# Kernel tuning notes

Hardware: AMD Instinct MI355X
Metric: run time of the kernel (lower is better)

## Reference

```python
import jax, jax.numpy as jnp
import numpy as np

D_FEAT = 6
HID = 256
T = 60
B_DAYS = 4
STOCKS = 512
TRAIN_DAYS = 240
K_DAY = 10
N_NEIGHBOR = 10
SLOPE = 0.01  # nn.LeakyReLU default


def setup_inputs() -> dict:
    key = jax.random.key(0)
    ks = jax.random.split(key, 32)
    g = lambda i, shape, s=0.05: (jax.random.normal(ks[i], shape, dtype=jnp.float32) * s)
    inp = jax.random.normal(ks[0], (B_DAYS, STOCKS, D_FEAT * T), dtype=jnp.float32)
    train_hidden = jax.random.normal(ks[1], (TRAIN_DAYS, STOCKS, HID), dtype=jnp.float32)
    train_hidden_day = jax.random.normal(ks[2], (TRAIN_DAYS, HID), dtype=jnp.float32)
    return {
        "inp": inp,
        "train_hidden": train_hidden,
        "train_hidden_day": train_hidden_day,
        # GRU layer 0 (input D_FEAT) and layer 1 (input HID); gates [r,z,n] stacked -> 3*HID
        "W_ih0": g(3, (3 * HID, D_FEAT)), "W_hh0": g(4, (3 * HID, HID)),
        "b_ih0": g(5, (3 * HID,)), "b_hh0": g(6, (3 * HID,)),
        "W_ih1": g(7, (3 * HID, HID)), "W_hh1": g(8, (3 * HID, HID)),
        "b_ih1": g(9, (3 * HID,)), "b_hh1": g(10, (3 * HID,)),
        # lins MLP 256->512->512->256
        "lin0_W": g(11, (512, HID)), "lin0_b": g(12, (512,)),
        "lin1_W": g(13, (512, 512)), "lin1_b": g(14, (512,)),
        "lin2_W": g(15, (HID, 512)), "lin2_b": g(16, (HID,)),
        # projections (no bias) and output head
        "proj1_W": g(17, (HID, HID)), "proj2_W": g(18, (HID, HID)),
        "fc_W": g(19, (1, 2 * HID)), "fc_b": g(20, (1,)),
    }


def _leaky(x):
    return jnp.where(x >= 0, x, SLOPE * x)


def _gru_layer(x, W_ih, W_hh, b_ih, b_hh):
    # x: [N, T, in] -> [N, T, HID]
    xW = jnp.einsum('nti,gi->ntg', x, W_ih) + b_ih  # precompute input gates
    def step(h, xw):
        gh = h @ W_hh.T + b_hh
        xr, xz, xn = jnp.split(xw, 3, axis=-1)
        hr, hz, hn = jnp.split(gh, 3, axis=-1)
        r = jax.nn.sigmoid(xr + hr)
        z = jax.nn.sigmoid(xz + hz)
        n = jnp.tanh(xn + r * hn)
        h = (1.0 - z) * n + z * h
        return h, h
    h0 = jnp.zeros((x.shape[0], W_hh.shape[1]), x.dtype)
    _, hs = jax.lax.scan(step, h0, jnp.swapaxes(xW, 0, 1))
    return jnp.swapaxes(hs, 0, 1)


def _cos_sim(x, y):
    xy = x @ y.T
    xn = jnp.sqrt(jnp.sum(x * x, axis=1))[:, None]
    yn = jnp.sqrt(jnp.sum(y * y, axis=1))[:, None]
    cs = xy / (xn @ yn.T)
    return jnp.where(jnp.isnan(cs), 0.0, cs)


def reference(inp, train_hidden, train_hidden_day,
              W_ih0, W_hh0, b_ih0, b_hh0, W_ih1, W_hh1, b_ih1, b_hh1,
              lin0_W, lin0_b, lin1_W, lin1_b, lin2_W, lin2_b,
              proj1_W, proj2_W, fc_W, fc_b):
    B, S = inp.shape[0], inp.shape[1]
    x = inp.reshape(B * S, D_FEAT, -1).transpose(0, 2, 1)  # [N, T, d_feat]
    h = _gru_layer(x, W_ih0, W_hh0, b_ih0, b_hh0)
    h = _gru_layer(h, W_ih1, W_hh1, b_ih1, b_hh1)
    out = h[:, -1, :]                                      # [N, HID]
    mb = _leaky(out @ lin0_W.T + lin0_b)
    mb = _leaky(mb @ lin1_W.T + lin1_b)
    mb = _leaky(mb @ lin2_W.T + lin2_b)                    # mini_batch_out [N, HID]
    mb_day = jnp.mean(mb.reshape(B, S, -1), axis=1)        # [B, HID]
    day_sim = _cos_sim(mb_day, train_hidden_day)           # [B, TRAIN_DAYS]
    _, day_idx = jax.lax.top_k(day_sim, K_DAY)             # [B, K_DAY]
    sample = train_hidden[day_idx].reshape(-1, train_hidden.shape[-1])  # [B*K_DAY*S, HID]
    q = mb @ proj1_W.T
    kh = sample @ proj2_W.T
    cs = _cos_sim(q, kh)                                   # [N, B*K_DAY*S]
    vals, idx = jax.lax.top_k(cs, N_NEIGHBOR)              # per-row top-k (distinct cols)
    # sparse mask (ones/n_neighbor) * cos_sim, then sparse @ kh == weighted gather-sum
    agg = jnp.einsum('nk,nkh->nh', vals / N_NEIGHBOR, kh[idx])
    cat = jnp.concatenate([mb, agg], axis=1)               # [N, 2*HID]
    y = (cat @ fc_W.T + fc_b).squeeze(-1)
    return y.reshape(B, -1)
```

## Files before the change

### kernel.cpp

```cpp
#include <hip/hip_runtime.h>
#include <cmath>
#include <cstdint>

#define D_FEAT 6
#define T_SEQ  60
#define HID    256
#define G3     768
#define NROW   2048
#define NSAMP  20480

__device__ __forceinline__ float sigmoidf_(float x) { return 1.0f / (1.0f + expf(-x)); }

struct PrepArgs {
  const float* src[9];
  float* dst[9];
  int N[9], K[9], ro[9];
};

__global__ void prep_weights(PrepArgs a) {
  int seg = blockIdx.y;
  const float* S = a.src[seg];
  float* D = a.dst[seg];
  int N = a.N[seg], K = a.K[seg], ro = a.ro[seg];
  int total = N * K;
  for (int i = blockIdx.x * blockDim.x + threadIdx.x; i < total; i += gridDim.x * blockDim.x) {
    int n = i / K, k = i - n * K;
    D[(size_t)(k + ro) * N + n] = S[i];
  }
}

__device__ __forceinline__ void kloop128(const float* __restrict__ A,
                                         const float* __restrict__ B,
                                         float (&acc)[3][8])
{
  float4 Aa[4][2];
  float  Bb[2][12];
#pragma unroll
  for (int c = 0; c < 4; ++c) {
    Aa[c][0] = *(const float4*)(A + c * 8);
    Aa[c][1] = *(const float4*)(A + c * 8 + 4);
  }
#pragma unroll
  for (int c = 0; c < 4; ++c)
#pragma unroll
    for (int u = 0; u < 3; ++u)
      Bb[0][c * 3 + u] = B[(size_t)c * G3 + u * 256];

  for (int kb = 0; kb < 128; kb += 8) {
    {
      const float* p = B + (size_t)(kb + 4) * G3;
#pragma unroll
      for (int c = 0; c < 4; ++c)
#pragma unroll
        for (int u = 0; u < 3; ++u)
          Bb[1][c * 3 + u] = p[(size_t)c * G3 + u * 256];
    }
#pragma unroll
    for (int c = 0; c < 4; ++c) {
      float4 alo = Aa[c][0], ahi = Aa[c][1];
      int kn = kb + 4 + c;
      Aa[c][0] = *(const float4*)(A + kn * 8);
      Aa[c][1] = *(const float4*)(A + kn * 8 + 4);
#pragma unroll
      for (int u = 0; u < 3; ++u) {
        float b = Bb[0][c * 3 + u];
        acc[u][0] += alo.x * b; acc[u][1] += alo.y * b;
        acc[u][2] += alo.z * b; acc[u][3] += alo.w * b;
        acc[u][4] += ahi.x * b; acc[u][5] += ahi.y * b;
        acc[u][6] += ahi.z * b; acc[u][7] += ahi.w * b;
      }
    }
    {
      int kw = (kb + 8) & 127;
      const float* p = B + (size_t)kw * G3;
#pragma unroll
      for (int c = 0; c < 4; ++c)
#pragma unroll
        for (int u = 0; u < 3; ++u)
          Bb[0][c * 3 + u] = p[(size_t)c * G3 + u * 256];
    }
#pragma unroll
    for (int c = 0; c < 4; ++c) {
      float4 alo = Aa[c][0], ahi = Aa[c][1];
      int kn = (kb + 8 + c) & 127;
      Aa[c][0] = *(const float4*)(A + kn * 8);
      Aa[c][1] = *(const float4*)(A + kn * 8 + 4);
#pragma unroll
      for (int u = 0; u < 3; ++u) {
        float b = Bb[1][c * 3 + u];
        acc[u][0] += alo.x * b; acc[u][1] += alo.y * b;
        acc[u][2] += alo.z * b; acc[u][3] += alo.w * b;
        acc[u][4] += ahi.x * b; acc[u][5] += ahi.y * b;
        acc[u][6] += ahi.z * b; acc[u][7] += ahi.w * b;
      }
    }
  }
}

__global__ __launch_bounds__(512, 1)
void gru_fused(const float* __restrict__ inp, const float* __restrict__ WThh0,
               const float* __restrict__ WTcat, const float* __restrict__ WTih0,
               const float* __restrict__ bih0, const float* __restrict__ bhh0,
               const float* __restrict__ bih1, const float* __restrict__ bhh1,
               float* __restrict__ hrow)
{
  __shared__ float h0A[2048], h0B[2048];
  __shared__ float h1A[2048], h1B[2048];
  __shared__ float xls[2880];
  __shared__ float exch[256 * 33];

  const int tid = threadIdx.x;
  const int col = tid & 255;
  const int half = tid >> 8;
  const int m0 = blockIdx.x * 8;

  for (int c = tid; c < 2880; c += 512) {
    int row = c / 360, it = c - row * 360;
    xls[it * 8 + row] = inp[(size_t)(m0 + row) * 360 + it];
  }
  for (int c = tid; c < 2048; c += 512) { h0A[c] = 0.f; h1A[c] = 0.f; }

  float h0c[8], h1c[8];
#pragma unroll
  for (int r = 0; r < 8; ++r) { h0c[r] = 0.f; h1c[r] = 0.f; }

  float b_ih0[3], b_hh0[3], b_ih1[3], b_hh1[3];
#pragma unroll
  for (int u = 0; u < 3; ++u) {
    int o = u * 256 + col;
    b_ih0[u] = bih0[o]; b_hh0[u] = bhh0[o];
    b_ih1[u] = bih1[o]; b_hh1[u] = bhh1[o];
  }
  __syncthreads();

  const int aoff = half * 1024;
  const float* Bhh0 = WThh0 + (size_t)(half * 128) * G3 + col;
  const float* Bc0  = WTcat + (size_t)(half * 128) * G3 + col;
  const float* Bc1  = WTcat + (size_t)(256 + half * 128) * G3 + col;
  float* exc = exch + col * 33;

  for (int t = 0; t < T_SEQ; ++t) {
    const float* h0cur = (t & 1) ? h0B : h0A;
    float*       h0nxt = (t & 1) ? h0A : h0B;
    const float* h1cur = (t & 1) ? h1B : h1A;
    float*       h1nxt = (t & 1) ? h1A : h1B;

    float gh[3][8];
#pragma unroll
    for (int u = 0; u < 3; ++u)
#pragma unroll
      for (int r = 0; r < 8; ++r) gh[u][r] = 0.f;
    kloop128(h0cur + aoff, Bhh0, gh);

    float xw[3][8];
    if (half == 0) {
#pragma unroll
      for (int u = 0; u < 3; ++u)
#pragma unroll
        for (int r = 0; r < 8; ++r) xw[u][r] = b_ih0[u];
#pragma unroll
      for (int i = 0; i < 6; ++i) {
        float4 xlo = *(const float4*)&xls[(i * 60 + t) * 8];
        float4 xhi = *(const float4*)&xls[(i * 60 + t) * 8 + 4];
#pragma unroll
        for (int u = 0; u < 3; ++u) {
          float b = WTih0[i * G3 + u * 256 + col];
          xw[u][0] += xlo.x * b; xw[u][1] += xlo.y * b;
          xw[u][2] += xlo.z * b; xw[u][3] += xlo.w * b;
          xw[u][4] += xhi.x * b; xw[u][5] += xhi.y * b;
          xw[u][6] += xhi.z * b; xw[u][7] += xhi.w * b;
        }
      }
    } else {
#pragma unroll
      for (int u = 0; u < 3; ++u)
#pragma unroll
        for (int r = 0; r < 8; ++r) exc[u * 8 + r] = gh[u][r];
    }
    __syncthreads();

    if (half == 0) {
      float hn[8];
#pragma unroll
      for (int r = 0; r < 8; ++r) {
        float g0 = gh[0][r] + exc[r];
        float g1 = gh[1][r] + exc[8 + r];
        float g2 = gh[2][r] + exc[16 + r];
        float rr = sigmoidf_(xw[0][r] + (g0 + b_hh0[0]));
        float zz = sigmoidf_(xw[1][r] + (g1 + b_hh0[1]));
        float nn = tanhf(xw[2][r] + rr * (g2 + b_hh0[2]));
        h0c[r] = (1.f - zz) * nn + zz * h0c[r];
        hn[r] = h0c[r];
      }
      *(float4*)&h0nxt[col * 8]     = *(float4*)&hn[0];
      *(float4*)&h0nxt[col * 8 + 4] = *(float4*)&hn[4];
    }
    __syncthreads();

    float acc[3][8];
#pragma unroll
    for (int u = 0; u < 3; ++u)
#pragma unroll
      for (int r = 0; r < 8; ++r) acc[u][r] = 0.f;
    kloop128(h0nxt + aoff, Bc0, acc);
    float xn8[8];
#pragma unroll
    for (int r = 0; r < 8; ++r) { xn8[r] = acc[2][r]; acc[2][r] = 0.f; }
    kloop128(h1cur + aoff, Bc1, acc);

    if (half == 1) {
#pragma unroll
      for (int r = 0; r < 8; ++r) {
        exc[r]      = acc[0][r];
        exc[8 + r]  = acc[1][r];
        exc[16 + r] = xn8[r];
        exc[24 + r] = acc[2][r];
      }
    }
    __syncthreads();

    if (half == 0) {
      float hn[8];
#pragma unroll
      for (int r = 0; r < 8; ++r) {
        float ra = acc[0][r] + exc[r];
        float za = acc[1][r] + exc[8 + r];
        float xa = xn8[r] + exc[16 + r];
        float ha = acc[2][r] + exc[24 + r];
        float rr = sigmoidf_((ra + b_ih1[0]) + b_hh1[0]);
        float zz = sigmoidf_((za + b_ih1[1]) + b_hh1[1]);
        float nn = tanhf((xa + b_ih1[2]) + rr * (ha + b_hh1[2]));
        h1c[r] = (1.f - zz) * nn + zz * h1c[r];
        hn[r] = h1c[r];
      }
      *(float4*)&h1nxt[col * 8]     = *(float4*)&hn[0];
      *(float4*)&h1nxt[col * 8 + 4] = *(float4*)&hn[4];
    }
    __syncthreads();
  }

  if (half == 0) {
#pragma unroll
    for (int r = 0; r < 8; ++r)
      hrow[(size_t)(m0 + r) * 256 + col] = h1c[r];
  }
}

__global__ __launch_bounds__(256, 2)
void gemm_act(const float* __restrict__ A, const int* __restrict__ rowsrc,
              const float* __restrict__ WT, const float* __restrict__ bias,
              float* __restrict__ C, int M, int N, int K, int act)
{
  __shared__ float4 As4[128 * 32];
  const int tx = threadIdx.x, ty = threadIdx.y;
  const int tid = ty * 32 + tx;
  const int n0 = blockIdx.x * 32, m0 = blockIdx.y * 32;
  const int K4 = K >> 2;

  for (int c = tid; c < K4 * 32; c += 256) {
    int k4 = c % K4, m = c / K4;
    int row = m0 + m;
    if (rowsrc) row = rowsrc[row];
    As4[k4 * 32 + m] = *(const float4*)(A + (size_t)row * K + k4 * 4);
  }
  __syncthreads();

  float acc[4] = {0,0,0,0};
  const int n = n0 + tx;
  const float* pb = WT + n;

  float bc[4], bn_[4];
#pragma unroll
  for (int kk = 0; kk < 4; ++kk) bc[kk] = pb[(size_t)kk * N];
  for (int k4 = 0; k4 < K4; ++k4) {
    int nk4 = (k4 + 1 < K4) ? (k4 + 1) : 0;
    const float* pn = pb + (size_t)nk4 * 4 * N;
#pragma unroll
    for (int kk = 0; kk < 4; ++kk) bn_[kk] = pn[(size_t)kk * N];
    float4 a0 = As4[k4 * 32 + ty * 4 + 0];
    float4 a1 = As4[k4 * 32 + ty * 4 + 1];
    float4 a2 = As4[k4 * 32 + ty * 4 + 2];
    float4 a3 = As4[k4 * 32 + ty * 4 + 3];
#pragma unroll
    for (int kk = 0; kk < 4; ++kk) {
      float b = bc[kk];
      acc[0] += ((const float*)&a0)[kk] * b;
      acc[1] += ((const float*)&a1)[kk] * b;
      acc[2] += ((const float*)&a2)[kk] * b;
      acc[3] += ((const float*)&a3)[kk] * b;
    }
#pragma unroll
    for (int q = 0; q < 4; ++q) bc[q] = bn_[q];
  }
  float bb = bias ? bias[n] : 0.f;
#pragma unroll
  for (int r = 0; r < 4; ++r) {
    float v = acc[r] + bb;
    if (act) v = (v >= 0.f) ? v : 0.01f * v;
    C[(size_t)(m0 + ty * 4 + r) * N + n] = v;
  }
}

__global__ void mbday_part(const float* __restrict__ mbf, float* __restrict__ part) {
  int d = blockIdx.x, sl = blockIdx.y, c = threadIdx.x;
  float s = 0.f;
  int base = d * 512 + sl * 64;
  for (int st = 0; st < 64; ++st) s += mbf[(size_t)(base + st) * 256 + c];
  part[(size_t)(d * 8 + sl) * 256 + c] = s;
}

__global__ void mbday_fin(const float* __restrict__ part, float* __restrict__ mbday) {
  int d = blockIdx.x, c = threadIdx.x;
  float s = 0.f;
#pragma unroll
  for (int p = 0; p < 8; ++p) s += part[(size_t)(d * 8 + p) * 256 + c];
  mbday[d * 256 + c] = s * (1.0f / 512.0f);
}

__global__ void daytopk_kernel(const float* __restrict__ mbday, const float* __restrict__ thd,
                               int* __restrict__ dayidx) {
  __shared__ float mbs[256];
  __shared__ float sim[256];
  __shared__ float red[256];
  __shared__ int   redi[256];
  const int d = blockIdx.x, t = threadIdx.x;
  mbs[t] = mbday[d * 256 + t];
  __syncthreads();
  red[t] = mbs[t] * mbs[t];
  __syncthreads();
  for (int o = 128; o; o >>= 1) { if (t < o) red[t] += red[t + o]; __syncthreads(); }
  float xn = sqrtf(red[0]);
  float v = -INFINITY;
  if (t < 240) {
    float dot = 0.f, yn2 = 0.f;
    for (int k = 0; k < 256; ++k) {
      float y = thd[t * 256 + k];
      dot += mbs[k] * y;
      yn2 += y * y;
    }
    float den = xn * sqrtf(yn2);
    v = (den > 0.f) ? dot / den : 0.f;
  }
  sim[t] = v;
  __syncthreads();
  for (int it = 0; it < 10; ++it) {
    red[t] = sim[t]; redi[t] = t;
    __syncthreads();
    for (int o = 128; o; o >>= 1) {
      if (t < o) {
        if (red[t + o] > red[t] || (red[t + o] == red[t] && redi[t + o] < redi[t])) {
          red[t] = red[t + o]; redi[t] = redi[t + o];
        }
      }
      __syncthreads();
    }
    if (t == 0) { int bi = redi[0]; dayidx[d * 10 + it] = bi; sim[bi] = -INFINITY; }
    __syncthreads();
  }
}

__global__ void rowsrc_kernel(const int* __restrict__ dayidx, int* __restrict__ rowsrc) {
  int r = blockIdx.x * 256 + threadIdx.x;
  if (r < NSAMP) rowsrc[r] = dayidx[r >> 9] * 512 + (r & 511);
}

__global__ void rownorm_kernel(const float* __restrict__ X, float* __restrict__ out, int rows) {
  int w = threadIdx.x >> 6;
  int lane = threadIdx.x & 63;
  int row = blockIdx.x * 4 + w;
  if (row >= rows) return;
  float4 x = *(const float4*)(X + (size_t)row * 256 + lane * 4);
  float s = x.x * x.x + x.y * x.y + x.z * x.z + x.w * x.w;
#pragma unroll
  for (int o = 32; o; o >>= 1) s += __shfl_down(s, o, 64);
  if (lane == 0) out[row] = sqrtf(s);
}

__global__ void qnorm_kernel(float* __restrict__ q, const float* __restrict__ qn) {
  int i = blockIdx.x * 256 + threadIdx.x;
  int row = i >> 8;
  float n = qn[row];
  q[i] = (n > 0.f) ? q[i] / n : 0.f;
}

__global__ void khT_kernel(const float* __restrict__ kh, const float* __restrict__ khn,
                           float* __restrict__ khT) {
  __shared__ float tile[32][33];
  int jb = blockIdx.x * 32;
  int kb = blockIdx.y * 32;
  int tx = threadIdx.x & 31, tyy = threadIdx.x >> 5;
  for (int rr = tyy; rr < 32; rr += 8) {
    float n = khn[jb + rr];
    float v = kh[(size_t)(jb + rr) * 256 + kb + tx];
    tile[rr][tx] = (n > 0.f) ? v / n : 0.f;
  }
  __syncthreads();
  for (int rr = tyy; rr < 32; rr += 8) {
    khT[(size_t)(kb + rr) * NSAMP + jb + tx] = tile[tx][rr];
  }
}

__global__ __launch_bounds__(256, 4)
void csmax_kernel(const float* __restrict__ qh, const float* __restrict__ khT,
                  float* __restrict__ topvp, int* __restrict__ topip)
{
  __shared__ float4 qs[256][2];
  __shared__ float csch[8 * 512];
  const int tid = threadIdx.x;
  const int split = blockIdx.x & 7;
  const int m0 = (blockIdx.x >> 3) * 8;
  {
    int k = tid;
    float4 v0, v1;
    v0.x = qh[(size_t)(m0 + 0) * 256 + k]; v0.y = qh[(size_t)(m0 + 1) * 256 + k];
    v0.z = qh[(size_t)(m0 + 2) * 256 + k]; v0.w = qh[(size_t)(m0 + 3) * 256 + k];
    v1.x = qh[(size_t)(m0 + 4) * 256 + k]; v1.y = qh[(size_t)(m0 + 5) * 256 + k];
    v1.z = qh[(size_t)(m0 + 6) * 256 + k]; v1.w = qh[(size_t)(m0 + 7) * 256 + k];
    qs[k][0] = v0; qs[k][1] = v1;
  }
  __syncthreads();
  const int lane = tid & 63;
  const int wv = tid >> 6;

  float tv0[10], tv1[10];
  int   tj0[10], tj1[10];
  int   tn0 = 0, tn1 = 0;
  float tmv0 = -INFINITY, tmv1 = -INFINITY;
  int   tmi0 = 0, tmi1 = 0;

  auto process_row = [&](int r, float (&tv)[10], int (&tj)[10], int& tn,
                         float& tmv, int& tmi, int jb) {
    float4 c0 = *(const float4*)&csch[r * 512 + lane * 8];
    float4 c1 = *(const float4*)&csch[r * 512 + lane * 8 + 4];
    float cv[8] = {c0.x, c0.y, c0.z, c0.w, c1.x, c1.y, c1.z, c1.w};
    const int cj0 = jb + lane * 8;
    while (true) {
      float bv = -INFINITY; int bj = 0x7fffffff;
#pragma unroll
      for (int u = 0; u < 8; ++u) {
        if (cv[u] > bv) { bv = cv[u]; bj = cj0 + u; }
      }
#pragma unroll
      for (int o = 32; o; o >>= 1) {
        float ov = __shfl_down(bv, o, 64);
        int   oj = __shfl_down(bj, o, 64);
        if (ov > bv || (ov == bv && oj < bj)) { bv = ov; bj = oj; }
      }
      bv = __shfl(bv, 0, 64); bj = __shfl(bj, 0, 64);
      bool take;
      if (tn < 10) take = true;
      else take = (bv > tmv) || (bv == tmv && bj < tmi);
      if (!take) break;
      if (tn < 10) {
#pragma unroll
        for (int s = 0; s < 10; ++s) if (s == tn) { tv[s] = bv; tj[s] = bj; }
        tn++;
        if (tn == 10) {
          float mv = tv[0]; int mi = tj[0];
#pragma unroll
          for (int s = 1; s < 10; ++s) {
            bool w = (tv[s] < mv) || (tv[s] == mv && tj[s] > mi);
            if (w) { mv = tv[s]; mi = tj[s]; }
          }
          tmv = mv; tmi = mi;
        }
      } else {
        int ms = 0; float mv = tv[0]; int mi = tj[0];
#pragma unroll
        for (int s = 1; s < 10; ++s) {
          bool w = (tv[s] < mv) || (tv[s] == mv && tj[s] > mi);
          if (w) { ms = s; mv = tv[s]; mi = tj[s]; }
        }
#pragma unroll
        for (int s = 0; s < 10; ++s) if (s == ms) { tv[s] = bv; tj[s] = bj; }
        mv = tv[0]; mi = tj[0];
#pragma unroll
        for (int s = 1; s < 10; ++s) {
          bool w = (tv[s] < mv) || (tv[s] == mv && tj[s] > mi);
          if (w) { mv = tv[s]; mi = tj[s]; }
        }
        tmv = mv; tmi = mi;
      }
#pragma unroll
      for (int u = 0; u < 8; ++u) if (cj0 + u == bj) cv[u] = -INFINITY;
    }
  };

  for (int ci = 0; ci < 5; ++ci) {
    const int ch = split * 5 + ci;
    const int jb = ch * 512;
    float acc[8][2];
#pragma unroll
    for (int r = 0; r < 8; ++r) { acc[r][0] = 0.f; acc[r][1] = 0.f; }
    const float* kp = khT + jb + tid;

    float b0c[4], b1c[4], b0n[4], b1n[4];
#pragma unroll
    for (int kk = 0; kk < 4; ++kk) {
      b0c[kk] = kp[(size_t)kk * NSAMP];
      b1c[kk] = kp[(size_t)kk * NSAMP + 256];
    }
    for (int k4 = 0; k4 < 64; ++k4) {
      int nk4 = (k4 + 1) & 63;
      const float* pn = kp + (size_t)nk4 * 4 * NSAMP;
#pragma unroll
      for (int kk = 0; kk < 4; ++kk) {
        b0n[kk] = pn[(size_t)kk * NSAMP];
        b1n[kk] = pn[(size_t)kk * NSAMP + 256];
      }
#pragma unroll
      for (int kk = 0; kk < 4; ++kk) {
        float4 qa = qs[k4 * 4 + kk][0];
        float4 qb = qs[k4 * 4 + kk][1];
        float b0 = b0c[kk], b1 = b1c[kk];
        acc[0][0] += qa.x * b0; acc[1][0] += qa.y * b0; acc[2][0] += qa.z * b0; acc[3][0] += qa.w * b0;
        acc[4][0] += qb.x * b0; acc[5][0] += qb.y * b0; acc[6][0] += qb.z * b0; acc[7][0] += qb.w * b0;
        acc[0][1] += qa.x * b1; acc[1][1] += qa.y * b1; acc[2][1] += qa.z * b1; acc[3][1] += qa.w * b1;
        acc[4][1] += qb.x * b1; acc[5][1] += qb.y * b1; acc[6][1] += qb.z * b1; acc[7][1] += qb.w * b1;
      }
#pragma unroll
      for (int q = 0; q < 4; ++q) { b0c[q] = b0n[q]; b1c[q] = b1n[q]; }
    }
    __syncthreads();
#pragma unroll
    for (int r = 0; r < 8; ++r) {
      csch[r * 512 + tid] = acc[r][0];
      csch[r * 512 + 256 + tid] = acc[r][1];
    }
    __syncthreads();
    process_row(wv,     tv0, tj0, tn0, tmv0, tmi0, jb);
    process_row(wv + 4, tv1, tj1, tn1, tmv1, tmi1, jb);
  }
  __syncthreads();

  if (lane == 0) {
    int row0 = m0 + wv;
#pragma unroll
    for (int s = 0; s < 10; ++s) {
      topvp[(size_t)row0 * 80 + split * 10 + s] = tv0[s];
      topip[(size_t)row0 * 80 + split * 10 + s] = tj0[s];
    }
    int row1 = m0 + wv + 4;
#pragma unroll
    for (int s = 0; s < 10; ++s) {
      topvp[(size_t)row1 * 80 + split * 10 + s] = tv1[s];
      topip[(size_t)row1 * 80 + split * 10 + s] = tj1[s];
    }
  }
}

__global__ void merge_topk(const float* __restrict__ topvp, const int* __restrict__ topip,
                           float* __restrict__ topv, int* __restrict__ topi)
{
  const int wv = threadIdx.x >> 6;
  const int lane = threadIdx.x & 63;
  const int row = blockIdx.x * 4 + wv;
  float v0 = topvp[(size_t)row * 80 + lane];
  int   i0 = topip[(size_t)row * 80 + lane];
  float v1 = (lane < 16) ? topvp[(size_t)row * 80 + 64 + lane] : -INFINITY;
  int   i1 = (lane < 16) ? topip[(size_t)row * 80 + 64 + lane] : 0x7fffffff;
  for (int s = 0; s < 10; ++s) {
    float bv = v0; int bj = i0;
    if (v1 > bv || (v1 == bv && i1 < bj)) { bv = v1; bj = i1; }
#pragma unroll
    for (int o = 1; o < 64; o <<= 1) {
      float ov = __shfl_xor(bv, o, 64);
      int   oj = __shfl_xor(bj, o, 64);
      if (ov > bv || (ov == bv && oj < bj)) { bv = ov; bj = oj; }
    }
    if (lane == 0) { topv[row * 10 + s] = bv; topi[row * 10 + s] = bj; }
    if (i0 == bj) { v0 = -INFINITY; i0 = 0x7fffffff; }
    if (i1 == bj) { v1 = -INFINITY; i1 = 0x7fffffff; }
  }
}

__global__ void final_kernel(const float* __restrict__ mb, const float* __restrict__ kh,
                             const float* __restrict__ topv, const int* __restrict__ topi,
                             const float* __restrict__ fcW, const float* __restrict__ fcb,
                             float* __restrict__ y)
{
  __shared__ float red[256];
  int n = blockIdx.x, c = threadIdx.x;
  float agg = 0.f;
#pragma unroll
  for (int k = 0; k < 10; ++k) {
    float w = topv[n * 10 + k] / 10.0f;
    int idx = topi[n * 10 + k];
    agg += w * kh[(size_t)idx * 256 + c];
  }
  float val = fcW[c] * mb[(size_t)n * 256 + c] + fcW[256 + c] * agg;
  red[c] = val;
  __syncthreads();
  for (int o = 128; o; o >>= 1) { if (c < o) red[c] += red[c + o]; __syncthreads(); }
  if (c == 0) y[n] = red[0] + fcb[0];
}

extern "C" void kernel_launch(void* const* d_in, const int* in_sizes, int n_in,
                              void* d_out, int out_size, void* d_ws, size_t ws_size,
                              hipStream_t stream)
{
  const float* inp    = (const float*)d_in[0];
  const float* trainh = (const float*)d_in[1];
  const float* thd    = (const float*)d_in[2];
  const float* Wih0   = (const float*)d_in[3];
  const float* Whh0   = (const float*)d_in[4];
  const float* bih0   = (const float*)d_in[5];
  const float* bhh0   = (const float*)d_in[6];
  const float* Wih1   = (const float*)d_in[7];
  const float* Whh1   = (const float*)d_in[8];
  const float* bih1   = (const float*)d_in[9];
  const float* bhh1   = (const float*)d_in[10];
  const float* lin0W  = (const float*)d_in[11];
  const float* lin0b  = (const float*)d_in[12];
  const float* lin1W  = (const float*)d_in[13];
  const float* lin1b  = (const float*)d_in[14];
  const float* lin2W  = (const float*)d_in[15];
  const float* lin2b  = (const float*)d_in[16];
  const float* p1W    = (const float*)d_in[17];
  const float* p2W    = (const float*)d_in[18];
  const float* fcW    = (const float*)d_in[19];
  const float* fcb    = (const float*)d_in[20];

  float* ws = (float*)d_ws;
  float* WT_hh0 = ws + 0;
  float* WTcat  = ws + 196608;
  float* WT_l0  = ws + 589824;
  float* WT_l1  = ws + 720896;
  float* WT_l2  = ws + 983040;
  float* WT_p1  = ws + 1114112;
  float* WT_p2  = ws + 1179648;
  float* hrow   = ws + 1245184;
  float* mb1    = ws + 3342336;
  float* mb2    = ws + 4390912;
  float* mbf    = ws + 5439488;
  float* mbday  = ws + 5963776;
  float* qbuf   = ws + 5964800;
  float* kh     = ws + 6489088;
  float* khT    = ws + 11731968;
  float* khn    = ws + 16974848;
  float* qn     = ws + 16995328;
  float* topv   = ws + 16997376;
  int*   dayidx = (int*)(ws + 17017856);
  int*   rowsrc = (int*)(ws + 17017920);
  int*   topi   = (int*)(ws + 17038400);
  float* topvp  = mb1;
  int*   topip  = (int*)(mb1 + 163840);
  float* WT_ih0 = mb2;
  float* mbpart = mb2;

  PrepArgs pa;
  pa.src[0] = Whh0;  pa.dst[0] = WT_hh0; pa.N[0] = 768; pa.K[0] = 256; pa.ro[0] = 0;
  pa.src[1] = Wih1;  pa.dst[1] = WTcat;  pa.N[1] = 768; pa.K[1] = 256; pa.ro[1] = 0;
  pa.src[2] = Whh1;  pa.dst[2] = WTcat;  pa.N[2] = 768; pa.K[2] = 256; pa.ro[2] = 256;
  pa.src[3] = lin0W; pa.dst[3] = WT_l0;  pa.N[3] = 512; pa.K[3] = 256; pa.ro[3] = 0;
  pa.src[4] = lin1W; pa.dst[4] = WT_l1;  pa.N[4] = 512; pa.K[4] = 512; pa.ro[4] = 0;
  pa.src[5] = lin2W; pa.dst[5] = WT_l2;  pa.N[5] = 256; pa.K[5] = 512; pa.ro[5] = 0;
  pa.src[6] = p1W;   pa.dst[6] = WT_p1;  pa.N[6] = 256; pa.K[6] = 256; pa.ro[6] = 0;
  pa.src[7] = p2W;   pa.dst[7] = WT_p2;  pa.N[7] = 256; pa.K[7] = 256; pa.ro[7] = 0;
  pa.src[8] = Wih0;  pa.dst[8] = WT_ih0; pa.N[8] = 768; pa.K[8] = 6;   pa.ro[8] = 0;
  prep_weights<<<dim3(64, 9), dim3(256), 0, stream>>>(pa);

  gru_fused<<<256, 512, 0, stream>>>(inp, WT_hh0, WTcat, WT_ih0, bih0, bhh0, bih1, bhh1, hrow);

  gemm_act<<<dim3(16, 64), dim3(32, 8), 0, stream>>>(hrow, nullptr, WT_l0, lin0b, mb1, 2048, 512, 256, 1);
  gemm_act<<<dim3(16, 64), dim3(32, 8), 0, stream>>>(mb1, nullptr, WT_l1, lin1b, mb2, 2048, 512, 512, 1);
  gemm_act<<<dim3(8, 64),  dim3(32, 8), 0, stream>>>(mb2, nullptr, WT_l2, lin2b, mbf, 2048, 256, 512, 1);

  mbday_part<<<dim3(4, 8), 256, 0, stream>>>(mbf, mbpart);
  mbday_fin<<<4, 256, 0, stream>>>(mbpart, mbday);
  daytopk_kernel<<<4, 256, 0, stream>>>(mbday, thd, dayidx);
  rowsrc_kernel<<<80, 256, 0, stream>>>(dayidx, rowsrc);

  gemm_act<<<dim3(8, 640), dim3(32, 8), 0, stream>>>(trainh, rowsrc, WT_p2, nullptr, kh, 20480, 256, 256, 0);
  gemm_act<<<dim3(8, 64),  dim3(32, 8), 0, stream>>>(mbf, nullptr, WT_p1, nullptr, qbuf, 2048, 256, 256, 0);

  rownorm_kernel<<<5120, 256, 0, stream>>>(kh, khn, 20480);
  rownorm_kernel<<<512, 256, 0, stream>>>(qbuf, qn, 2048);
  qnorm_kernel<<<2048, 256, 0, stream>>>(qbuf, qn);
  khT_kernel<<<dim3(640, 8), 256, 0, stream>>>(kh, khn, khT);

  csmax_kernel<<<2048, 256, 0, stream>>>(qbuf, khT, topvp, topip);
  merge_topk<<<512, 256, 0, stream>>>(topvp, topip, topv, topi);
  final_kernel<<<2048, 256, 0, stream>>>(mbf, kh, topv, topi, fcW, fcb, (float*)d_out);

  (void)in_sizes; (void)n_in; (void)out_size; (void)ws_size;
}
```

Baseline: 3.326 ms.

## Split GRU K-reduction four ways with 1024-thread blocks and packed weights

The fused GRU kernel now uses 1024 threads per block instead of 512, splitting each recurrent matmul's K dimension into four 64-wide slices rather than two 128-wide slices. Every quarter now computes the gate nonlinearities for 2 of the 8 rows after an all-to-all exchange through a larger shared buffer, so gate work is no longer serialized on one half. GRU weights are repacked into a K-by-4 interleaved layout so each thread loads float4 vectors of B instead of scalars. This aims to shorten the per-timestep serial critical path, at the cost of more shared-memory exchange traffic and more register pressure per thread.

```diff
diff --git a/kernel.cpp b/kernel.cpp
--- a/kernel.cpp
+++ b/kernel.cpp
@@ -14,46 +14,52 @@
 struct PrepArgs {
   const float* src[9];
   float* dst[9];
-  int N[9], K[9], ro[9];
+  int N[9], K[9], ro[9], pk[9];
 };
 
 __global__ void prep_weights(PrepArgs a) {
   int seg = blockIdx.y;
   const float* S = a.src[seg];
   float* D = a.dst[seg];
-  int N = a.N[seg], K = a.K[seg], ro = a.ro[seg];
+  int N = a.N[seg], K = a.K[seg], ro = a.ro[seg], pk = a.pk[seg];
   int total = N * K;
   for (int i = blockIdx.x * blockDim.x + threadIdx.x; i < total; i += gridDim.x * blockDim.x) {
     int n = i / K, k = i - n * K;
-    D[(size_t)(k + ro) * N + n] = S[i];
-  }
-}
-
-__device__ __forceinline__ void kloop128(const float* __restrict__ A,
-                                         const float* __restrict__ B,
-                                         float (&acc)[3][8])
+    if (pk) {
+      int u = n >> 8, cn = n & 255;
+      int kg = k + ro;
+      D[(size_t)((kg >> 2) * 3 + u) * 1024 + cn * 4 + (kg & 3)] = S[i];
+    } else {
+      D[(size_t)(k + ro) * N + n] = S[i];
+    }
+  }
+}
+
+#define FMA8(alo, ahi, b, accrow) \
+  accrow[0] += alo.x * (b); accrow[1] += alo.y * (b); accrow[2] += alo.z * (b); accrow[3] += alo.w * (b); \
+  accrow[4] += ahi.x * (b); accrow[5] += ahi.y * (b); accrow[6] += ahi.z * (b); accrow[7] += ahi.w * (b);
+
+__device__ __forceinline__ void kloop64(const float* __restrict__ A,
+                                        const float* __restrict__ B,
+                                        float (&acc)[3][8])
 {
   float4 Aa[4][2];
-  float  Bb[2][12];
+  float Ba[3][4], Bb[3][4];
 #pragma unroll
   for (int c = 0; c < 4; ++c) {
     Aa[c][0] = *(const float4*)(A + c * 8);
     Aa[c][1] = *(const float4*)(A + c * 8 + 4);
   }
 #pragma unroll
-  for (int c = 0; c < 4; ++c)
-#pragma unroll
-    for (int u = 0; u < 3; ++u)
-      Bb[0][c * 3 + u] = B[(size_t)c * G3 + u * 256];
-
-  for (int kb = 0; kb < 128; kb += 8) {
+  for (int u = 0; u < 3; ++u)
+    *(float4*)Ba[u] = *(const float4*)(B + u * 1024);
+
+  for (int kb = 0; kb < 64; kb += 8) {
     {
-      const float* p = B + (size_t)(kb + 4) * G3;
-#pragma unroll
-      for (int c = 0; c < 4; ++c)
-#pragma unroll
-        for (int u = 0; u < 3; ++u)
-          Bb[1][c * 3 + u] = p[(size_t)c * G3 + u * 256];
+      const float* p = B + (size_t)(kb / 4 + 1) * 3072;
+#pragma unroll
+      for (int u = 0; u < 3; ++u)
+        *(float4*)Bb[u] = *(const float4*)(p + u * 1024);
     }
 #pragma unroll
     for (int c = 0; c < 4; ++c) {
@@ -61,45 +67,32 @@
       int kn = kb + 4 + c;
       Aa[c][0] = *(const float4*)(A + kn * 8);
       Aa[c][1] = *(const float4*)(A + kn * 8 + 4);
-#pragma unroll
-      for (int u = 0; u < 3; ++u) {
-        float b = Bb[0][c * 3 + u];
-        acc[u][0] += alo.x * b; acc[u][1] += alo.y * b;
-        acc[u][2] += alo.z * b; acc[u][3] += alo.w * b;
-        acc[u][4] += ahi.x * b; acc[u][5] += ahi.y * b;
-        acc[u][6] += ahi.z * b; acc[u][7] += ahi.w * b;
-      }
+      FMA8(alo, ahi, Ba[0][c], acc[0]);
+      FMA8(alo, ahi, Ba[1][c], acc[1]);
+      FMA8(alo, ahi, Ba[2][c], acc[2]);
     }
     {
-      int kw = (kb + 8) & 127;
-      const float* p = B + (size_t)kw * G3;
-#pragma unroll
-      for (int c = 0; c < 4; ++c)
-#pragma unroll
-        for (int u = 0; u < 3; ++u)
-          Bb[0][c * 3 + u] = p[(size_t)c * G3 + u * 256];
+      const float* p = B + (size_t)((kb / 4 + 2) & 15) * 3072;
+#pragma unroll
+      for (int u = 0; u < 3; ++u)
+        *(float4*)Ba[u] = *(const float4*)(p + u * 1024);
     }
 #pragma unroll
     for (int c = 0; c < 4; ++c) {
       float4 alo = Aa[c][0], ahi = Aa[c][1];
-      int kn = (kb + 8 + c) & 127;
+      int kn = (kb + 8 + c) & 63;
       Aa[c][0] = *(const float4*)(A + kn * 8);
       Aa[c][1] = *(const float4*)(A + kn * 8 + 4);
-#pragma unroll
-      for (int u = 0; u < 3; ++u) {
-        float b = Bb[1][c * 3 + u];
-        acc[u][0] += alo.x * b; acc[u][1] += alo.y * b;
-        acc[u][2] += alo.z * b; acc[u][3] += alo.w * b;
-        acc[u][4] += ahi.x * b; acc[u][5] += ahi.y * b;
-        acc[u][6] += ahi.z * b; acc[u][7] += ahi.w * b;
-      }
-    }
-  }
-}
-
-__global__ __launch_bounds__(512, 1)
-void gru_fused(const float* __restrict__ inp, const float* __restrict__ WThh0,
-               const float* __restrict__ WTcat, const float* __restrict__ WTih0,
+      FMA8(alo, ahi, Bb[0][c], acc[0]);
+      FMA8(alo, ahi, Bb[1][c], acc[1]);
+      FMA8(alo, ahi, Bb[2][c], acc[2]);
+    }
+  }
+}
+
+__global__ __launch_bounds__(1024, 4)
+void gru_fused(const float* __restrict__ inp, const float* __restrict__ Whh0p,
+               const float* __restrict__ Wcatp, const float* __restrict__ WTih0,
                const float* __restrict__ bih0, const float* __restrict__ bhh0,
                const float* __restrict__ bih1, const float* __restrict__ bhh1,
                float* __restrict__ hrow)
@@ -107,22 +100,21 @@
   __shared__ float h0A[2048], h0B[2048];
   __shared__ float h1A[2048], h1B[2048];
   __shared__ float xls[2880];
-  __shared__ float exch[256 * 33];
+  __shared__ float exch[256 * 97];
 
   const int tid = threadIdx.x;
   const int col = tid & 255;
-  const int half = tid >> 8;
-  const int m0 = blockIdx.x * 8;
-
-  for (int c = tid; c < 2880; c += 512) {
+  const int q   = tid >> 8;
+  const int m0  = blockIdx.x * 8;
+  const int r0  = q * 2;
+
+  for (int c = tid; c < 2880; c += 1024) {
     int row = c / 360, it = c - row * 360;
     xls[it * 8 + row] = inp[(size_t)(m0 + row) * 360 + it];
   }
-  for (int c = tid; c < 2048; c += 512) { h0A[c] = 0.f; h1A[c] = 0.f; }
-
-  float h0c[8], h1c[8];
-#pragma unroll
-  for (int r = 0; r < 8; ++r) { h0c[r] = 0.f; h1c[r] = 0.f; }
+  for (int c = tid; c < 2048; c += 1024) { h0A[c] = 0.f; h1A[c] = 0.f; }
+
+  float h0c[2] = {0.f, 0.f}, h1c[2] = {0.f, 0.f};
 
   float b_ih0[3], b_hh0[3], b_ih1[3], b_hh1[3];
 #pragma unroll
@@ -133,11 +125,11 @@
   }
   __syncthreads();
 
-  const int aoff = half * 1024;
-  const float* Bhh0 = WThh0 + (size_t)(half * 128) * G3 + col;
-  const float* Bc0  = WTcat + (size_t)(half * 128) * G3 + col;
-  const float* Bc1  = WTcat + (size_t)(256 + half * 128) * G3 + col;
-  float* exc = exch + col * 33;
+  const int aoff = q << 9;
+  const float* Bhh = Whh0p + (size_t)(q * 16) * 3072 + col * 4;
+  const float* Bc0 = Wcatp + (size_t)(q * 16) * 3072 + col * 4;
+  const float* Bc1 = Wcatp + (size_t)(64 + q * 16) * 3072 + col * 4;
+  float* exc = exch + col * 97;
 
   for (int t = 0; t < T_SEQ; ++t) {
     const float* h0cur = (t & 1) ? h0B : h0A;
@@ -150,50 +142,54 @@
     for (int u = 0; u < 3; ++u)
 #pragma unroll
       for (int r = 0; r < 8; ++r) gh[u][r] = 0.f;
-    kloop128(h0cur + aoff, Bhh0, gh);
-
-    float xw[3][8];
-    if (half == 0) {
-#pragma unroll
-      for (int u = 0; u < 3; ++u)
-#pragma unroll
-        for (int r = 0; r < 8; ++r) xw[u][r] = b_ih0[u];
-#pragma unroll
-      for (int i = 0; i < 6; ++i) {
-        float4 xlo = *(const float4*)&xls[(i * 60 + t) * 8];
-        float4 xhi = *(const float4*)&xls[(i * 60 + t) * 8 + 4];
+    kloop64(h0cur + aoff, Bhh, gh);
+
+    float xw[2][3];
+#pragma unroll
+    for (int r2 = 0; r2 < 2; ++r2)
+#pragma unroll
+      for (int u = 0; u < 3; ++u) xw[r2][u] = b_ih0[u];
+#pragma unroll
+    for (int i = 0; i < 6; ++i) {
+      float x0 = xls[(i * 60 + t) * 8 + r0];
+      float x1 = xls[(i * 60 + t) * 8 + r0 + 1];
+#pragma unroll
+      for (int u = 0; u < 3; ++u) {
+        float b = WTih0[i * G3 + u * 256 + col];
+        xw[0][u] += x0 * b;
+        xw[1][u] += x1 * b;
+      }
+    }
+#pragma unroll
+    for (int p = 0; p < 4; ++p) {
+      if (p == q) continue;
+      int qrel = (q < p) ? q : q - 1;
+#pragma unroll
+      for (int u = 0; u < 3; ++u) {
+        exc[((p * 3 + qrel) * 3 + u) * 2 + 0] = gh[u][p * 2 + 0];
+        exc[((p * 3 + qrel) * 3 + u) * 2 + 1] = gh[u][p * 2 + 1];
+      }
+    }
+    __syncthreads();
+    {
+      float g[3][2];
+#pragma unroll
+      for (int u = 0; u < 3; ++u) { g[u][0] = gh[u][r0]; g[u][1] = gh[u][r0 + 1]; }
+#pragma unroll
+      for (int qs = 0; qs < 3; ++qs)
 #pragma unroll
         for (int u = 0; u < 3; ++u) {
-          float b = WTih0[i * G3 + u * 256 + col];
-          xw[u][0] += xlo.x * b; xw[u][1] += xlo.y * b;
-          xw[u][2] += xlo.z * b; xw[u][3] += xlo.w * b;
-          xw[u][4] += xhi.x * b; xw[u][5] += xhi.y * b;
-          xw[u][6] += xhi.z * b; xw[u][7] += xhi.w * b;
+          g[u][0] += exc[((q * 3 + qs) * 3 + u) * 2 + 0];
+          g[u][1] += exc[((q * 3 + qs) * 3 + u) * 2 + 1];
         }
-      }
-    } else {
-#pragma unroll
-      for (int u = 0; u < 3; ++u)
-#pragma unroll
-        for (int r = 0; r < 8; ++r) exc[u * 8 + r] = gh[u][r];
-    }
-    __syncthreads();
-
-    if (half == 0) {
-      float hn[8];
-#pragma unroll
-      for (int r = 0; r < 8; ++r) {
-        float g0 = gh[0][r] + exc[r];
-        float g1 = gh[1][r] + exc[8 + r];
-        float g2 = gh[2][r] + exc[16 + r];
-        float rr = sigmoidf_(xw[0][r] + (g0 + b_hh0[0]));
-        float zz = sigmoidf_(xw[1][r] + (g1 + b_hh0[1]));
-        float nn = tanhf(xw[2][r] + rr * (g2 + b_hh0[2]));
-        h0c[r] = (1.f - zz) * nn + zz * h0c[r];
-        hn[r] = h0c[r];
-      }
-      *(float4*)&h0nxt[col * 8]     = *(float4*)&hn[0];
-      *(float4*)&h0nxt[col * 8 + 4] = *(float4*)&hn[4];
+#pragma unroll
+      for (int r2 = 0; r2 < 2; ++r2) {
+        float rr = sigmoidf_(xw[r2][0] + (g[0][r2] + b_hh0[0]));
+        float zz = sigmoidf_(xw[r2][1] + (g[1][r2] + b_hh0[1]));
+        float nn = tanhf(xw[r2][2] + rr * (g[2][r2] + b_hh0[2]));
+        h0c[r2] = (1.f - zz) * nn + zz * h0c[r2];
+        h0nxt[col * 8 + r0 + r2] = h0c[r2];
+      }
     }
     __syncthreads();
 
@@ -202,48 +198,59 @@
     for (int u = 0; u < 3; ++u)
 #pragma unroll
       for (int r = 0; r < 8; ++r) acc[u][r] = 0.f;
-    kloop128(h0nxt + aoff, Bc0, acc);
+    kloop64(h0nxt + aoff, Bc0, acc);
     float xn8[8];
 #pragma unroll
     for (int r = 0; r < 8; ++r) { xn8[r] = acc[2][r]; acc[2][r] = 0.f; }
-    kloop128(h1cur + aoff, Bc1, acc);
-
-    if (half == 1) {
-#pragma unroll
-      for (int r = 0; r < 8; ++r) {
-        exc[r]      = acc[0][r];
-        exc[8 + r]  = acc[1][r];
-        exc[16 + r] = xn8[r];
-        exc[24 + r] = acc[2][r];
-      }
-    }
-    __syncthreads();
-
-    if (half == 0) {
-      float hn[8];
-#pragma unroll
-      for (int r = 0; r < 8; ++r) {
-        float ra = acc[0][r] + exc[r];
-        float za = acc[1][r] + exc[8 + r];
-        float xa = xn8[r] + exc[16 + r];
-        float ha = acc[2][r] + exc[24 + r];
-        float rr = sigmoidf_((ra + b_ih1[0]) + b_hh1[0]);
-        float zz = sigmoidf_((za + b_ih1[1]) + b_hh1[1]);
-        float nn = tanhf((xa + b_ih1[2]) + rr * (ha + b_hh1[2]));
-        h1c[r] = (1.f - zz) * nn + zz * h1c[r];
-        hn[r] = h1c[r];
-      }
-      *(float4*)&h1nxt[col * 8]     = *(float4*)&hn[0];
-      *(float4*)&h1nxt[col * 8 + 4] = *(float4*)&hn[4];
-    }
-    __syncthreads();
-  }
-
-  if (half == 0) {
-#pragma unroll
-    for (int r = 0; r < 8; ++r)
-      hrow[(size_t)(m0 + r) * 256 + col] = h1c[r];
-  }
+    kloop64(h1cur + aoff, Bc1, acc);
+
+#pragma unroll
+    for (int p = 0; p < 4; ++p) {
+      if (p == q) continue;
+      int qrel = (q < p) ? q : q - 1;
+      int base = (p * 3 + qrel) * 8;
+#pragma unroll
+      for (int r2 = 0; r2 < 2; ++r2) {
+        exc[base + 0 + r2] = acc[0][p * 2 + r2];
+        exc[base + 2 + r2] = acc[1][p * 2 + r2];
+        exc[base + 4 + r2] = xn8[p * 2 + r2];
+        exc[base + 6 + r2] = acc[2][p * 2 + r2];
+      }
+    }
+    __syncthreads();
+    {
+      float R[2], Z[2], XN[2], HN[2];
+#pragma unroll
+      for (int r2 = 0; r2 < 2; ++r2) {
+        R[r2] = acc[0][r0 + r2]; Z[r2] = acc[1][r0 + r2];
+        XN[r2] = xn8[r0 + r2];   HN[r2] = acc[2][r0 + r2];
+      }
+#pragma unroll
+      for (int qs = 0; qs < 3; ++qs) {
+        int base = (q * 3 + qs) * 8;
+#pragma unroll
+        for (int r2 = 0; r2 < 2; ++r2) {
+          R[r2]  += exc[base + 0 + r2];
+          Z[r2]  += exc[base + 2 + r2];
+          XN[r2] += exc[base + 4 + r2];
+          HN[r2] += exc[base + 6 + r2];
+        }
+      }
+#pragma unroll
+      for (int r2 = 0; r2 < 2; ++r2) {
+        float rr = sigmoidf_((R[r2] + b_ih1[0]) + b_hh1[0]);
+        float zz = sigmoidf_((Z[r2] + b_ih1[1]) + b_hh1[1]);
+        float nn = tanhf((XN[r2] + b_ih1[2]) + rr * (HN[r2] + b_hh1[2]));
+        h1c[r2] = (1.f - zz) * nn + zz * h1c[r2];
+        h1nxt[col * 8 + r0 + r2] = h1c[r2];
+      }
+    }
+    __syncthreads();
+  }
+
+#pragma unroll
+  for (int r2 = 0; r2 < 2; ++r2)
+    hrow[(size_t)(m0 + r0 + r2) * 256 + col] = h1c[r2];
 }
 
 __global__ __launch_bounds__(256, 2)
@@ -290,7 +297,7 @@
       acc[3] += ((const float*)&a3)[kk] * b;
     }
 #pragma unroll
-    for (int q = 0; q < 4; ++q) bc[q] = bn_[q];
+    for (int qq = 0; qq < 4; ++qq) bc[qq] = bn_[qq];
   }
   float bb = bias ? bias[n] : 0.f;
 #pragma unroll
@@ -519,7 +526,7 @@
         acc[4][1] += qb.x * b1; acc[5][1] += qb.y * b1; acc[6][1] += qb.z * b1; acc[7][1] += qb.w * b1;
       }
 #pragma unroll
-      for (int q = 0; q < 4; ++q) { b0c[q] = b0n[q]; b1c[q] = b1n[q]; }
+      for (int qq = 0; qq < 4; ++qq) { b0c[qq] = b0n[qq]; b1c[qq] = b1n[qq]; }
     }
     __syncthreads();
 #pragma unroll
@@ -649,18 +656,18 @@
   float* mbpart = mb2;
 
   PrepArgs pa;
-  pa.src[0] = Whh0;  pa.dst[0] = WT_hh0; pa.N[0] = 768; pa.K[0] = 256; pa.ro[0] = 0;
-  pa.src[1] = Wih1;  pa.dst[1] = WTcat;  pa.N[1] = 768; pa.K[1] = 256; pa.ro[1] = 0;
-  pa.src[2] = Whh1;  pa.dst[2] = WTcat;  pa.N[2] = 768; pa.K[2] = 256; pa.ro[2] = 256;
-  pa.src[3] = lin0W; pa.dst[3] = WT_l0;  pa.N[3] = 512; pa.K[3] = 256; pa.ro[3] = 0;
-  pa.src[4] = lin1W; pa.dst[4] = WT_l1;  pa.N[4] = 512; pa.K[4] = 512; pa.ro[4] = 0;
-  pa.src[5] = lin2W; pa.dst[5] = WT_l2;  pa.N[5] = 256; pa.K[5] = 512; pa.ro[5] = 0;
-  pa.src[6] = p1W;   pa.dst[6] = WT_p1;  pa.N[6] = 256; pa.K[6] = 256; pa.ro[6] = 0;
-  pa.src[7] = p2W;   pa.dst[7] = WT_p2;  pa.N[7] = 256; pa.K[7] = 256; pa.ro[7] = 0;
-  pa.src[8] = Wih0;  pa.dst[8] = WT_ih0; pa.N[8] = 768; pa.K[8] = 6;   pa.ro[8] = 0;
+  pa.src[0] = Whh0;  pa.dst[0] = WT_hh0; pa.N[0] = 768; pa.K[0] = 256; pa.ro[0] = 0;   pa.pk[0] = 1;
+  pa.src[1] = Wih1;  pa.dst[1] = WTcat;  pa.N[1] = 768; pa.K[1] = 256; pa.ro[1] = 0;   pa.pk[1] = 1;
+  pa.src[2] = Whh1;  pa.dst[2] = WTcat;  pa.N[2] = 768; pa.K[2] = 256; pa.ro[2] = 256; pa.pk[2] = 1;
+  pa.src[3] = lin0W; pa.dst[3] = WT_l0;  pa.N[3] = 512; pa.K[3] = 256; pa.ro[3] = 0;   pa.pk[3] = 0;
+  pa.src[4] = lin1W; pa.dst[4] = WT_l1;  pa.N[4] = 512; pa.K[4] = 512; pa.ro[4] = 0;   pa.pk[4] = 0;
+  pa.src[5] = lin2W; pa.dst[5] = WT_l2;  pa.N[5] = 256; pa.K[5] = 512; pa.ro[5] = 0;   pa.pk[5] = 0;
+  pa.src[6] = p1W;   pa.dst[6] = WT_p1;  pa.N[6] = 256; pa.K[6] = 256; pa.ro[6] = 0;   pa.pk[6] = 0;
+  pa.src[7] = p2W;   pa.dst[7] = WT_p2;  pa.N[7] = 256; pa.K[7] = 256; pa.ro[7] = 0;   pa.pk[7] = 0;
+  pa.src[8] = Wih0;  pa.dst[8] = WT_ih0; pa.N[8] = 768; pa.K[8] = 6;   pa.ro[8] = 0;   pa.pk[8] = 0;
   prep_weights<<<dim3(64, 9), dim3(256), 0, stream>>>(pa);
 
-  gru_fused<<<256, 512, 0, stream>>>(inp, WT_hh0, WTcat, WT_ih0, bih0, bhh0, bih1, bhh1, hrow);
+  gru_fused<<<256, 1024, 0, stream>>>(inp, WT_hh0, WTcat, WT_ih0, bih0, bhh0, bih1, bhh1, hrow);
 
   gemm_act<<<dim3(16, 64), dim3(32, 8), 0, stream>>>(hrow, nullptr, WT_l0, lin0b, mb1, 2048, 512, 256, 1);
   gemm_act<<<dim3(16, 64), dim3(32, 8), 0, stream>>>(mb1, nullptr, WT_l1, lin1b, mb2, 2048, 512, 512, 1);
```

New measurement: 4.277 ms. 1.29x slower.
